# Kernel tuning notes

Measured on AMD Instinct MI355X. Metric: run time of the kernel, lower is better.

The kernel has to match this reference:

```python
import jax, jax.numpy as jnp
import numpy as np

B, S, D = 2, 2048, 2048
N_HEADS, N_KV_HEADS, HEAD_DIM = 16, 8, 128
N_REP = N_HEADS // N_KV_HEADS
EPS = 1e-6
SCALE = HEAD_DIM ** -0.5


def setup_inputs() -> dict:
    key = jax.random.key(0)
    ks = jax.random.split(key, 6)
    x = jax.random.normal(ks[0], (B, S, D), dtype=jnp.float32)
    # RoPE frequencies (Llama-style cis stored as interleaved [cos, sin])
    inv_freq = 1.0 / (1e6 ** (jnp.arange(0, HEAD_DIM, 2, dtype=jnp.float32) / HEAD_DIM))
    angles = jnp.arange(S, dtype=jnp.float32)[:, None] * inv_freq[None, :]  # [S, HEAD_DIM//2]
    freqs_cis = jnp.stack([jnp.cos(angles), jnp.sin(angles)], axis=-1)  # [S, HEAD_DIM//2, 2]
    wq = jax.random.normal(ks[1], (N_HEADS * HEAD_DIM, D), dtype=jnp.float32) * 0.02
    wk = jax.random.normal(ks[2], (N_KV_HEADS * HEAD_DIM, D), dtype=jnp.float32) * 0.02
    wv = jax.random.normal(ks[3], (N_KV_HEADS * HEAD_DIM, D), dtype=jnp.float32) * 0.02
    wo = jax.random.normal(ks[4], (D, N_HEADS * HEAD_DIM), dtype=jnp.float32) * 0.02
    q_norm_w = jnp.ones((HEAD_DIM,), dtype=jnp.float32)
    k_norm_w = jnp.ones((HEAD_DIM,), dtype=jnp.float32)
    return {"x": x, "freqs_cis": freqs_cis, "wq": wq, "wk": wk, "wv": wv,
            "wo": wo, "q_norm_w": q_norm_w, "k_norm_w": k_norm_w}


def _rmsnorm(t, w):
    var = jnp.mean(jnp.square(t), axis=-1, keepdims=True)
    return t * jax.lax.rsqrt(var + EPS) * w


def _apply_rope(t, cos, sin):
    # t: [B, S, H, HEAD_DIM]; cos/sin: [1, S, 1, HEAD_DIM//2]
    tp = t.reshape(*t.shape[:-1], HEAD_DIM // 2, 2)
    tr, ti = tp[..., 0], tp[..., 1]
    out = jnp.stack([tr * cos - ti * sin, tr * sin + ti * cos], axis=-1)
    return out.reshape(t.shape)


def reference(x, freqs_cis, wq, wk, wv, wo, q_norm_w, k_norm_w):
    bs, seqlen, _ = x.shape
    xq = (x @ wq.T).reshape(bs, seqlen, N_HEADS, HEAD_DIM)
    xk = (x @ wk.T).reshape(bs, seqlen, N_KV_HEADS, HEAD_DIM)
    xv = (x @ wv.T).reshape(bs, seqlen, N_KV_HEADS, HEAD_DIM)
    # per-head RMSNorm (Qwen3)
    xq = _rmsnorm(xq, q_norm_w)
    xk = _rmsnorm(xk, k_norm_w)
    # rotary embedding
    cos = freqs_cis[:seqlen, :, 0][None, :, None, :]
    sin = freqs_cis[:seqlen, :, 1][None, :, None, :]
    xq = _apply_rope(xq, cos, sin)
    xk = _apply_rope(xk, cos, sin)
    # GQA: repeat kv heads
    keys = jnp.repeat(xk, N_REP, axis=2)    # [B, S, N_HEADS, HEAD_DIM]
    values = jnp.repeat(xv, N_REP, axis=2)
    q = xq.transpose(0, 2, 1, 3)   # [B, H, S, D]
    k = keys.transpose(0, 2, 1, 3)
    v = values.transpose(0, 2, 1, 3)
    scores = jnp.einsum("bhqd,bhkd->bhqk", q, k) * SCALE
    causal = jnp.tril(jnp.ones((seqlen, seqlen), dtype=bool))
    scores = jnp.where(causal[None, None], scores, jnp.finfo(scores.dtype).min)
    attn = jax.nn.softmax(scores, axis=-1)
    out = jnp.einsum("bhqk,bhkd->bhqd", attn, v)
    out = out.transpose(0, 2, 1, 3).reshape(bs, seqlen, N_HEADS * HEAD_DIM)
    return out @ wo.T
```

## Files before the change

kernel.cpp:

```cpp
#include <hip/hip_runtime.h>

#define B_ 2
#define S_ 2048
#define D_ 2048
#define NH 16
#define NKV 8
#define HD 128
#define SCALE 0.08838834764831845f
#define CEXP 0.1275255f
#define RTHR 62.733f

typedef unsigned short u16;
typedef __attribute__((ext_vector_type(8))) short short8;
typedef __attribute__((ext_vector_type(4))) float f32x4;
typedef __attribute__((ext_vector_type(16))) float f32x16;
typedef __attribute__((ext_vector_type(4))) int i32x4;
typedef __attribute__((ext_vector_type(2))) int i32x2;

#define ASM_VMCNT(N) asm volatile("s_waitcnt vmcnt(" #N ")" ::: "memory")
#define LGKM0_FENCE asm volatile("s_waitcnt lgkmcnt(0)" ::: "memory")
#define MEMFENCE asm volatile("" ::: "memory")

__device__ __forceinline__ u16 f2b(float f) {
  union { float f; unsigned u; } c; c.f = f;
  unsigned u = c.u;
  return (u16)((u + 0x7fffu + ((u >> 16) & 1u)) >> 16);
}
__device__ __forceinline__ float b2f(u16 h) {
  union { unsigned u; float f; } c; c.u = ((unsigned)h) << 16;
  return c.f;
}
__device__ __forceinline__ float exp2f_fast(float x) {
  float r; asm("v_exp_f32 %0, %1" : "=v"(r) : "v"(x)); return r;
}
__device__ __forceinline__ int cvtpk(float a, float b) {
  int r; asm("v_cvt_pk_bf16_f32 %0, %1, %2" : "=v"(r) : "v"(a), "v"(b)); return r;
}
__device__ __forceinline__ void pl32swap(int& a, int& b) {
  asm volatile("v_permlane32_swap_b32 %0, %1" : "+v"(a), "+v"(b));
}

__device__ __forceinline__ void load_lds16(const u16* g, u16* l) {
  __builtin_amdgcn_global_load_lds(
      (const __attribute__((address_space(1))) unsigned int*)g,
      (__attribute__((address_space(3))) unsigned int*)l, 16, 0, 0);
}

__global__ __launch_bounds__(256) void cvt_all(const float* __restrict__ x,
                                               const float* __restrict__ wq,
                                               const float* __restrict__ wk,
                                               const float* __restrict__ wv,
                                               const float* __restrict__ wo,
                                               u16* __restrict__ xb,
                                               u16* __restrict__ wqkvb,
                                               u16* __restrict__ wob) {
  const int blk = blockIdx.x;
  const float* src; u16* dst; int base;
  if (blk < 8192)       { src = x;  dst = xb;                  base = blk; }
  else if (blk < 12288) { src = wq; dst = wqkvb;               base = blk - 8192; }
  else if (blk < 14336) { src = wk; dst = wqkvb + 2048 * 2048; base = blk - 12288; }
  else if (blk < 16384) { src = wv; dst = wqkvb + 3072 * 2048; base = blk - 14336; }
  else                  { src = wo; dst = wob;                 base = blk - 16384; }
  int i = base * 256 + threadIdx.x;
  float4 v = ((const float4*)src)[i];
  u16 o0 = f2b(v.x), o1 = f2b(v.y), o2 = f2b(v.z), o3 = f2b(v.w);
  unsigned long long packed = (unsigned long long)o0 | ((unsigned long long)o1 << 16) |
                              ((unsigned long long)o2 << 32) | ((unsigned long long)o3 << 48);
  ((unsigned long long*)dst)[i] = packed;
}

#define LDA4(dst, SRC, MI0) \
  { _Pragma("unroll") for (int i2 = 0; i2 < 4; ++i2) { \
      const int arow = wr * 128 + (MI0 + i2) * 16 + r; \
      dst[i2] = *(const short8*)&(SRC)[arow * 32 + ((hi ^ ((arow >> 1) & 3)) << 3)]; } }
#define LDB4(dst, SRC) \
  { _Pragma("unroll") for (int n2 = 0; n2 < 4; ++n2) { \
      const int brow = wc * 64 + n2 * 16 + r; \
      dst[n2] = *(const short8*)&(SRC)[brow * 32 + ((hi ^ ((brow >> 1) & 3)) << 3)]; } }
#define MFMA16(MI0, AF, BF) \
  { __builtin_amdgcn_s_setprio(1); \
    _Pragma("unroll") for (int i2 = 0; i2 < 4; ++i2) \
    _Pragma("unroll") for (int n2 = 0; n2 < 4; ++n2) \
      acc[MI0 + i2][n2] = __builtin_amdgcn_mfma_f32_16x16x32_bf16(AF[i2], BF[n2], acc[MI0 + i2][n2], 0, 0, 0); \
    __builtin_amdgcn_s_setprio(0); }

template<int OUTF32>
__global__ __launch_bounds__(512, 2) void gemm256(const u16* __restrict__ A, const u16* __restrict__ Bm,
                                                  void* __restrict__ Cv, int M, int N, int K, int nbn) {
  __shared__ __align__(16) u16 As[2][2][8192];
  __shared__ __align__(16) u16 Bs[2][2][8192];
  const int tid = threadIdx.x;
  const int wave = tid >> 6, lane = tid & 63;
  const int cpx = gridDim.x >> 3;
  const int L = (blockIdx.x & 7) * cpx + (blockIdx.x >> 3);
  const int bm = L / nbn, bn = L % nbn;
  const int wr = wave >> 2, wc = wave & 3;
  const int r = lane & 15, hi = lane >> 4;
  const int rowA0 = bm * 256, rowB0 = bn * 256;

  f32x4 acc[8][4];
#pragma unroll
  for (int mi = 0; mi < 8; ++mi)
#pragma unroll
    for (int ni = 0; ni < 4; ++ni) acc[mi][ni] = (f32x4){0.f, 0.f, 0.f, 0.f};

  auto stage_half = [&](const u16* G, int rowbase, u16* ldsb, int kcol) {
#pragma unroll
    for (int l = 0; l < 2; ++l) {
      const int p = wave * 2048 + l * 1024 + lane * 16;
      const int row = p >> 6, slot = (p >> 4) & 3;
      const int kg = slot ^ ((row >> 1) & 3);
      load_lds16(G + (size_t)(rowbase + row) * K + kcol + kg * 8,
                 ldsb + ((wave * 2048 + l * 1024) >> 1));
    }
  };

  stage_half(A,  rowA0, &As[0][0][0], 0);
  stage_half(Bm, rowB0, &Bs[0][0][0], 0);
  stage_half(A,  rowA0, &As[0][1][0], 32);
  stage_half(Bm, rowB0, &Bs[0][1][0], 32);
  ASM_VMCNT(4);
  __builtin_amdgcn_s_barrier();
  MEMFENCE;

  const int nk = K >> 6;
  for (int kt = 0; kt < nk; ++kt) {
    const int c = kt & 1, nb2 = c ^ 1;
    const int kn = (kt + 1) << 6;
    const bool hn = kt + 1 < nk;
    const u16* a0 = As[c][0]; const u16* b0 = Bs[c][0];
    const u16* a1 = As[c][1]; const u16* b1 = Bs[c][1];
    short8 af[4], bf[4];
    LDB4(bf, b0); LDA4(af, a0, 0);
    if (hn) stage_half(A, rowA0, &As[nb2][0][0], kn);
    __builtin_amdgcn_s_barrier();
    LGKM0_FENCE;
    MFMA16(0, af, bf);
    MEMFENCE;
    __builtin_amdgcn_s_barrier();
    LDA4(af, a0, 4);
    if (hn) { stage_half(Bm, rowB0, &Bs[nb2][0][0], kn); ASM_VMCNT(4); }
    else    { ASM_VMCNT(0); }
    __builtin_amdgcn_s_barrier();
    LGKM0_FENCE;
    MFMA16(4, af, bf);
    MEMFENCE;
    __builtin_amdgcn_s_barrier();
    LDB4(bf, b1); LDA4(af, a1, 0);
    if (hn) stage_half(A, rowA0, &As[nb2][1][0], kn + 32);
    __builtin_amdgcn_s_barrier();
    LGKM0_FENCE;
    MFMA16(0, af, bf);
    MEMFENCE;
    __builtin_amdgcn_s_barrier();
    LDA4(af, a1, 4);
    if (hn) { stage_half(Bm, rowB0, &Bs[nb2][1][0], kn + 32); ASM_VMCNT(4); }
    __builtin_amdgcn_s_barrier();
    LGKM0_FENCE;
    MFMA16(4, af, bf);
    MEMFENCE;
    __builtin_amdgcn_s_barrier();
  }

#pragma unroll
  for (int mi = 0; mi < 8; ++mi)
#pragma unroll
    for (int ni = 0; ni < 4; ++ni)
#pragma unroll
      for (int r2 = 0; r2 < 4; ++r2) {
        int grow = bm * 256 + wr * 128 + mi * 16 + hi * 4 + r2;
        int gcol = bn * 256 + wc * 64 + ni * 16 + r;
        if (OUTF32)
          ((float*)Cv)[(size_t)grow * N + gcol] = acc[mi][ni][r2];
        else
          ((u16*)Cv)[(size_t)grow * N + gcol] = f2b(acc[mi][ni][r2]);
      }
}

template<int OUTF32>
__global__ __launch_bounds__(256, 2) void gemm_bt2(const u16* __restrict__ A, const u16* __restrict__ Bm,
                                                   void* __restrict__ Cv, int M, int N, int K, int nbn) {
  __shared__ __align__(16) u16 As[2][128 * 64];
  __shared__ __align__(16) u16 Bs[2][128 * 64];
  const int tid = threadIdx.x;
  const int wave = tid >> 6, lane = tid & 63;
  const int nwg = gridDim.x, cpx = nwg >> 3;
  const int L = (blockIdx.x & 7) * cpx + (blockIdx.x >> 3);
  const int bm = L / nbn, bn = L % nbn;
  const int wr = wave >> 1, wc = wave & 1;
  const int r = lane & 15, hi = lane >> 4;

  f32x4 acc[4][4];
#pragma unroll
  for (int m = 0; m < 4; ++m)
#pragma unroll
    for (int n = 0; n < 4; ++n) acc[m][n] = (f32x4){0.f, 0.f, 0.f, 0.f};

  const int gslot = (lane & 7) ^ (lane >> 3);
  const int srow = lane >> 3;

  auto stage = [&](int buf, int k0) {
#pragma unroll
    for (int jj = 0; jj < 4; ++jj) {
      int j = wave * 4 + jj;
      int row = j * 8 + srow;
      load_lds16(A + (size_t)(bm * 128 + row) * K + k0 + gslot * 8, &As[buf][j * 512]);
      load_lds16(Bm + (size_t)(bn * 128 + row) * K + k0 + gslot * 8, &Bs[buf][j * 512]);
    }
  };

  const int nk = K >> 6;
  stage(0, 0);
  for (int kt = 0; kt < nk; ++kt) {
    if (kt + 1 < nk) {
      stage((kt + 1) & 1, (kt + 1) << 6);
      ASM_VMCNT(8);
    } else {
      ASM_VMCNT(0);
    }
    __builtin_amdgcn_s_barrier();
    MEMFENCE;
    const u16* as = As[kt & 1];
    const u16* bs = Bs[kt & 1];
#pragma unroll
    for (int kc = 0; kc < 2; ++kc) {
      short8 af[4], bfr[4];
#pragma unroll
      for (int m = 0; m < 4; ++m) {
        int row = wr * 64 + m * 16 + r;
        int slot = (hi + kc * 4) ^ (row & 7);
        af[m] = *(const short8*)&as[row * 64 + slot * 8];
      }
#pragma unroll
      for (int n = 0; n < 4; ++n) {
        int row = wc * 64 + n * 16 + r;
        int slot = (hi + kc * 4) ^ (row & 7);
        bfr[n] = *(const short8*)&bs[row * 64 + slot * 8];
      }
#pragma unroll
      for (int m = 0; m < 4; ++m)
#pragma unroll
        for (int n = 0; n < 4; ++n)
          acc[m][n] = __builtin_amdgcn_mfma_f32_16x16x32_bf16(af[m], bfr[n], acc[m][n], 0, 0, 0);
    }
    MEMFENCE;
    __builtin_amdgcn_s_barrier();
  }

#pragma unroll
  for (int m = 0; m < 4; ++m)
#pragma unroll
    for (int n = 0; n < 4; ++n)
#pragma unroll
      for (int r2 = 0; r2 < 4; ++r2) {
        int grow = bm * 128 + wr * 64 + m * 16 + hi * 4 + r2;
        int gcol = bn * 128 + wc * 64 + n * 16 + r;
        if (OUTF32)
          ((float*)Cv)[(size_t)grow * N + gcol] = acc[m][n][r2];
        else
          ((u16*)Cv)[(size_t)grow * N + gcol] = f2b(acc[m][n][r2]);
      }
}

__global__ __launch_bounds__(256) void rmsnorm_rope(const u16* __restrict__ qkv, const float* __restrict__ fc,
                                                    const float* __restrict__ qw, const float* __restrict__ kw,
                                                    u16* __restrict__ qr, u16* __restrict__ kr) {
  const int tid = threadIdx.x, wave = tid >> 6, lane = tid & 63;
  const int rowid = blockIdx.x * 4 + wave;
  const int token = rowid / 24;
  const int hh = rowid % 24;
  const int b = token >> 11, s = token & 2047;
  const bool isq = hh < 16;
  const int off = isq ? hh * 128 : 2048 + (hh - 16) * 128;
  const u16* src = qkv + (size_t)token * 4096 + off + lane * 2;
  unsigned pv = *(const unsigned*)src;
  float t0 = b2f((u16)(pv & 0xffffu));
  float t1 = b2f((u16)(pv >> 16));
  float ss = t0 * t0 + t1 * t1;
#pragma unroll
  for (int mm = 1; mm < 64; mm <<= 1) ss += __shfl_xor(ss, mm, 64);
  float rms = rsqrtf(ss * (1.0f / 128.0f) + 1e-6f);
  const float* nw = isq ? qw : kw;
  t0 *= rms * nw[lane * 2];
  t1 *= rms * nw[lane * 2 + 1];
  float c = fc[(s * 64 + lane) * 2], sn = fc[(s * 64 + lane) * 2 + 1];
  float o0 = t0 * c - t1 * sn;
  float o1 = t0 * sn + t1 * c;
  unsigned ov = (unsigned)f2b(o0) | ((unsigned)f2b(o1) << 16);
  if (isq)
    *(unsigned*)(qr + ((size_t)(b * 16 + hh) * 2048 + s) * 128 + lane * 2) = ov;
  else
    *(unsigned*)(kr + ((size_t)(b * 8 + hh - 16) * 2048 + s) * 128 + lane * 2) = ov;
}

__global__ __launch_bounds__(256) void v_transpose(const u16* __restrict__ qkv, u16* __restrict__ vt) {
  __shared__ __align__(16) u16 tile[64][136];
  const int blk = blockIdx.x;
  const int st = blk & 31, h = (blk >> 5) & 7, b = blk >> 8;
  const int s0 = st * 64, t = threadIdx.x;
#pragma unroll
  for (int p = 0; p < 4; ++p) {
    int row = p * 16 + (t >> 4), c8 = (t & 15) * 8;
    const u16* src = qkv + (size_t)(b * 2048 + s0 + row) * 4096 + 3072 + h * 128 + c8;
    *(short8*)&tile[row][c8] = *(const short8*)src;
  }
  __syncthreads();
  const int d = t >> 1, j0 = (t & 1) * 32;
  u16* dst = vt + ((size_t)(b * 8 + h) * 128 + d) * 2048 + s0 + j0;
#pragma unroll
  for (int j = 0; j < 32; j += 8) {
    short8 v;
#pragma unroll
    for (int u = 0; u < 8; ++u) v[u] = (short)tile[j0 + j + u][d];
    *(short8*)(dst + j) = v;
  }
}

__global__ __launch_bounds__(256, 2) void attn7(const u16* __restrict__ qr, const u16* __restrict__ kr,
                                                const u16* __restrict__ vt, u16* __restrict__ ao) {
  __shared__ __align__(16) u16 Ks[2][64 * 128];
  __shared__ __align__(16) u16 Vs[2][128 * 64];
  const int tid = threadIdx.x, wave = tid >> 6, lane = tid & 63;
  const int ql = lane & 31, lh = lane >> 5;

  const int blk = blockIdx.x;
  const int half = blk >> 8;
  const int xcd = blk & 7;
  const int idx = (blk >> 3) & 31;
  const int bh = xcd * 4 + (idx & 3);
  const int pp = idx >> 2;
  const int t = half ? pp : 15 - pp;
  const int b = bh >> 4, h = bh & 15, hkv = h >> 1;

  const u16* Q  = qr + (size_t)(b * 16 + h) * S_ * HD;
  const u16* Kg = kr + (size_t)(b * 8 + hkv) * S_ * HD;
  const u16* Vg = vt + (size_t)(b * 8 + hkv) * HD * S_;

  const int q0w = t * 128 + wave * 32;
  const int nsteps = 2 * (t + 1);

  short8 qf[8];
#pragma unroll
  for (int ki = 0; ki < 8; ++ki)
    qf[ki] = *(const short8*)(Q + (size_t)(q0w + ql) * HD + ki * 16 + lh * 8);

  f32x16 o[4];
#pragma unroll
  for (int dt = 0; dt < 4; ++dt) o[dt] = 0.f;
  float m = -1e30f, l = 0.f;

  auto stage = [&](int buf, int kv0) {
#pragma unroll
    for (int inst = 0; inst < 4; ++inst) {
      int pp2 = wave * 4096 + inst * 1024 + lane * 16;
      int row = pp2 >> 8;
      int colb = (pp2 & 255) ^ ((row & 7) << 4);
      load_lds16(Kg + (((size_t)(kv0 + row)) << 7) + (colb >> 1),
                 &Ks[buf][(wave * 4096 + inst * 1024) >> 1]);
    }
#pragma unroll
    for (int inst = 0; inst < 4; ++inst) {
      int pp2 = wave * 4096 + inst * 1024 + lane * 16;
      int d = pp2 >> 7;
      int colb = (pp2 & 127) ^ ((d & 7) << 4);
      load_lds16(Vg + (size_t)d * S_ + kv0 + (colb >> 1),
                 &Vs[buf][(wave * 4096 + inst * 1024) >> 1]);
    }
  };

  stage(0, 0);
  for (int i = 0; i < nsteps; ++i) {
    const int kv0 = i * 64;
    const u16* kb = Ks[i & 1];
    const u16* vb = Vs[i & 1];
    if (i + 1 < nsteps) {
      stage((i + 1) & 1, kv0 + 64);
      ASM_VMCNT(8);
    } else {
      ASM_VMCNT(0);
    }
    __builtin_amdgcn_s_barrier();
    MEMFENCE;

    if (kv0 < q0w + 32) {
      f32x16 sacc[2];
      sacc[0] = 0.f; sacc[1] = 0.f;
      __builtin_amdgcn_s_setprio(1);
#pragma unroll
      for (int ki = 0; ki < 8; ++ki) {
        const int off = ki * 32 + lh * 16;
#pragma unroll
        for (int kvt = 0; kvt < 2; ++kvt) {
          const int row = kvt * 32 + ql;
          short8 kf = *(const short8*)&kb[(row << 7) + ((off ^ ((row & 7) << 4)) >> 1)];
          sacc[kvt] = __builtin_amdgcn_mfma_f32_32x32x16_bf16(kf, qf[ki], sacc[kvt], 0, 0, 0);
        }
      }
      __builtin_amdgcn_s_setprio(0);
      const int q = q0w + ql;
      if (kv0 + 64 > q0w) {
#pragma unroll
        for (int kvt = 0; kvt < 2; ++kvt) {
          const int kvb = kv0 + kvt * 32 + 4 * lh;
#pragma unroll
          for (int reg = 0; reg < 16; ++reg) {
            const int kvr = kvb + (reg & 3) + 8 * (reg >> 2);
            sacc[kvt][reg] = (kvr > q) ? -1e30f : sacc[kvt][reg];
          }
        }
      }
      float mx = sacc[0][0];
#pragma unroll
      for (int kvt = 0; kvt < 2; ++kvt)
#pragma unroll
        for (int reg = 0; reg < 16; ++reg) mx = fmaxf(mx, sacc[kvt][reg]);
      mx = fmaxf(mx, __shfl_xor(mx, 32, 64));
      if (__any(mx > m + RTHR)) {
        float mn = fmaxf(m, mx);
        float sc = exp2f_fast((m - mn) * CEXP);
        l *= sc;
        m = mn;
#pragma unroll
        for (int dt = 0; dt < 4; ++dt)
#pragma unroll
          for (int reg = 0; reg < 16; ++reg) o[dt][reg] *= sc;
      }
      short8 pf[4];
      const float mc = m * CEXP;
      float ps = 0.f;
#pragma unroll
      for (int kvt = 0; kvt < 2; ++kvt) {
        float pv[16];
#pragma unroll
        for (int reg = 0; reg < 16; ++reg) {
          pv[reg] = exp2f_fast(__builtin_fmaf(sacc[kvt][reg], CEXP, -mc));
          ps += pv[reg];
        }
        int A0 = cvtpk(pv[0], pv[1]),  B0 = cvtpk(pv[2], pv[3]);
        int C0 = cvtpk(pv[4], pv[5]),  D0 = cvtpk(pv[6], pv[7]);
        int A1 = cvtpk(pv[8], pv[9]),  B1 = cvtpk(pv[10], pv[11]);
        int C1 = cvtpk(pv[12], pv[13]), D1 = cvtpk(pv[14], pv[15]);
        pl32swap(A0, C0);
        pl32swap(B0, D0);
        pl32swap(A1, C1);
        pl32swap(B1, D1);
        i32x4 w0 = (i32x4){A0, B0, C0, D0};
        i32x4 w1 = (i32x4){A1, B1, C1, D1};
        pf[kvt * 2]     = *(short8*)&w0;
        pf[kvt * 2 + 1] = *(short8*)&w1;
      }
      l += ps;
      __builtin_amdgcn_s_setprio(1);
#pragma unroll
      for (int kc = 0; kc < 4; ++kc) {
        const int off = kc * 32 + lh * 16;
#pragma unroll
        for (int dt = 0; dt < 4; ++dt) {
          const int d = dt * 32 + ql;
          short8 vf = *(const short8*)&vb[(d << 6) + ((off ^ ((d & 7) << 4)) >> 1)];
          o[dt] = __builtin_amdgcn_mfma_f32_32x32x16_bf16(vf, pf[kc], o[dt], 0, 0, 0);
        }
      }
      __builtin_amdgcn_s_setprio(0);
    }
    MEMFENCE;
    __builtin_amdgcn_s_barrier();
  }

  l += __shfl_xor(l, 32, 64);
  const float inv = 1.0f / l;
  const size_t rowoff = ((size_t)(b * 2048 + q0w + ql)) * 2048 + h * 128;
#pragma unroll
  for (int dt = 0; dt < 4; ++dt)
#pragma unroll
    for (int g = 0; g < 4; ++g) {
      const int d0 = dt * 32 + 8 * g + 4 * lh;
      int w0 = cvtpk(o[dt][4 * g] * inv, o[dt][4 * g + 1] * inv);
      int w1 = cvtpk(o[dt][4 * g + 2] * inv, o[dt][4 * g + 3] * inv);
      i32x2 pk = (i32x2){w0, w1};
      *(i32x2*)((u16*)ao + rowoff + d0) = pk;
    }
}

extern "C" void kernel_launch(void* const* d_in, const int* in_sizes, int n_in,
                              void* d_out, int out_size, void* d_ws, size_t ws_size,
                              hipStream_t stream) {
  const float* x = (const float*)d_in[0];
  const float* fc = (const float*)d_in[1];
  const float* wq = (const float*)d_in[2];
  const float* wk = (const float*)d_in[3];
  const float* wv = (const float*)d_in[4];
  const float* wo = (const float*)d_in[5];
  const float* qw = (const float*)d_in[6];
  const float* kw = (const float*)d_in[7];
  float* out = (float*)d_out;
  char* ws = (char*)d_ws;

  u16* xb    = (u16*)(ws);
  u16* wqkvb = (u16*)(ws + 16777216);
  u16* wob   = (u16*)(ws + 33554432);
  u16* qkv   = (u16*)(ws + 41943040);
  u16* qrope = (u16*)(ws + 75497472);
  u16* krope = (u16*)(ws + 92274688);
  u16* vtb   = (u16*)(ws + 100663296);
  u16* ao    = (u16*)(ws + 109051904);

  cvt_all<<<20480, 256, 0, stream>>>(x, wq, wk, wv, wo, xb, wqkvb, wob);

  gemm256<0><<<256, 512, 0, stream>>>(xb, wqkvb, (void*)qkv, 4096, 4096, 2048, 16);

  rmsnorm_rope<<<24576, 256, 0, stream>>>(qkv, fc, qw, kw, qrope, krope);
  v_transpose<<<512, 256, 0, stream>>>(qkv, vtb);

  attn7<<<512, 256, 0, stream>>>(qrope, krope, vtb, ao);

  gemm_bt2<1><<<512, 256, 0, stream>>>(ao, wob, (void*)out, 4096, 2048, 2048, 16);
}
```

Baseline: 211.5 us.

## Double-buffer GEMM register fragments to overlap LDS reads with MFMA

Restructures the GEMM main loop to use separate even/odd register fragment sets, so LDS reads for the next MFMA phase are issued before the current MFMA block runs. The explicit lgkmcnt(0) waits are removed and global-load waits are re-tuned, which shortens the chain of barrier-separated stalls. The cost is more register pressure, and the code now relies on the compiler to insert correct LDS wait counts. Reordering the stage_half calls also changes which buffer halves are in flight at each barrier, so correctness depends on the vmcnt values being right.

```diff
diff --git a/kernel.cpp b/kernel.cpp
--- a/kernel.cpp
+++ b/kernel.cpp
@@ -18,7 +18,6 @@
 typedef __attribute__((ext_vector_type(2))) int i32x2;
 
 #define ASM_VMCNT(N) asm volatile("s_waitcnt vmcnt(" #N ")" ::: "memory")
-#define LGKM0_FENCE asm volatile("s_waitcnt lgkmcnt(0)" ::: "memory")
 #define MEMFENCE asm volatile("" ::: "memory")
 
 __device__ __forceinline__ u16 f2b(float f) {
@@ -123,41 +122,46 @@
   __builtin_amdgcn_s_barrier();
   MEMFENCE;
 
+  short8 afE[4], afO[4], bfE[4], bfO[4];
+  LDB4(bfE, Bs[0][0]);
+  LDA4(afE, As[0][0], 0);
+
   const int nk = K >> 6;
   for (int kt = 0; kt < nk; ++kt) {
     const int c = kt & 1, nb2 = c ^ 1;
     const int kn = (kt + 1) << 6;
     const bool hn = kt + 1 < nk;
-    const u16* a0 = As[c][0]; const u16* b0 = Bs[c][0];
-    const u16* a1 = As[c][1]; const u16* b1 = Bs[c][1];
-    short8 af[4], bf[4];
-    LDB4(bf, b0); LDA4(af, a0, 0);
-    if (hn) stage_half(A, rowA0, &As[nb2][0][0], kn);
-    __builtin_amdgcn_s_barrier();
-    LGKM0_FENCE;
-    MFMA16(0, af, bf);
-    MEMFENCE;
-    __builtin_amdgcn_s_barrier();
-    LDA4(af, a0, 4);
-    if (hn) { stage_half(Bm, rowB0, &Bs[nb2][0][0], kn); ASM_VMCNT(4); }
+    LDA4(afO, As[c][0], 4);
+    if (hn) { stage_half(A, rowA0, &As[nb2][0][0], kn); ASM_VMCNT(2); }
     else    { ASM_VMCNT(0); }
-    __builtin_amdgcn_s_barrier();
-    LGKM0_FENCE;
-    MFMA16(4, af, bf);
-    MEMFENCE;
-    __builtin_amdgcn_s_barrier();
-    LDB4(bf, b1); LDA4(af, a1, 0);
-    if (hn) stage_half(A, rowA0, &As[nb2][1][0], kn + 32);
-    __builtin_amdgcn_s_barrier();
-    LGKM0_FENCE;
-    MFMA16(0, af, bf);
-    MEMFENCE;
-    __builtin_amdgcn_s_barrier();
-    LDA4(af, a1, 4);
-    if (hn) { stage_half(Bm, rowB0, &Bs[nb2][1][0], kn + 32); ASM_VMCNT(4); }
-    __builtin_amdgcn_s_barrier();
-    LGKM0_FENCE;
-    MFMA16(4, af, bf);
+    MEMFENCE;
+    __builtin_amdgcn_s_barrier();
+    MFMA16(0, afE, bfE);
+    MEMFENCE;
+    __builtin_amdgcn_s_barrier();
+    LDA4(afE, As[c][1], 0);
+    LDB4(bfO, Bs[c][1]);
+    if (hn) stage_half(Bm, rowB0, &Bs[nb2][0][0], kn);
+    MEMFENCE;
+    __builtin_amdgcn_s_barrier();
+    MFMA16(4, afO, bfE);
+    MEMFENCE;
+    __builtin_amdgcn_s_barrier();
+    LDA4(afO, As[c][1], 4);
+    if (hn) { stage_half(A, rowA0, &As[nb2][1][0], kn + 32); ASM_VMCNT(2); }
+    MEMFENCE;
+    __builtin_amdgcn_s_barrier();
+    MFMA16(0, afE, bfO);
+    MEMFENCE;
+    __builtin_amdgcn_s_barrier();
+    if (hn) {
+      LDA4(afE, As[nb2][0], 0);
+      LDB4(bfE, Bs[nb2][0]);
+      stage_half(Bm, rowB0, &Bs[nb2][1][0], kn + 32);
+    }
+    MEMFENCE;
+    __builtin_amdgcn_s_barrier();
+    MFMA16(4, afO, bfO);
     MEMFENCE;
     __builtin_amdgcn_s_barrier();
   }
```

Result: slower. 216.7 us (+2.4%).

## Replace QKV GEMM with 256x128-tile single-buffered kernel at higher occupancy

Applied to the files above, without the earlier changes.

The QKV projection GEMM changes from 256x256 tiles with a double-buffered, barrier-interleaved pipeline to 256x128 tiles over 512 blocks. Each k-step loads both 32-wide halves, waits on vmcnt(0), then runs the MFMAs. The smaller accumulator and LDS footprint allow launch bounds of 4 blocks per CU, and latency hiding is meant to come from other resident blocks rather than in-block prefetch. The cost is losing the global-load/compute overlap inside a block and more redundant A-tile loads.

```diff
diff --git a/kernel.cpp b/kernel.cpp
--- a/kernel.cpp
+++ b/kernel.cpp
@@ -18,7 +18,6 @@
 typedef __attribute__((ext_vector_type(2))) int i32x2;
 
 #define ASM_VMCNT(N) asm volatile("s_waitcnt vmcnt(" #N ")" ::: "memory")
-#define LGKM0_FENCE asm volatile("s_waitcnt lgkmcnt(0)" ::: "memory")
 #define MEMFENCE asm volatile("" ::: "memory")
 
 __device__ __forceinline__ u16 f2b(float f) {
@@ -69,111 +68,85 @@
   ((unsigned long long*)dst)[i] = packed;
 }
 
-#define LDA4(dst, SRC, MI0) \
+#define LDA4Q(dst, SRC) \
   { _Pragma("unroll") for (int i2 = 0; i2 < 4; ++i2) { \
-      const int arow = wr * 128 + (MI0 + i2) * 16 + r; \
+      const int arow = wr * 64 + i2 * 16 + r; \
       dst[i2] = *(const short8*)&(SRC)[arow * 32 + ((hi ^ ((arow >> 1) & 3)) << 3)]; } }
-#define LDB4(dst, SRC) \
+#define LDB4Q(dst, SRC) \
   { _Pragma("unroll") for (int n2 = 0; n2 < 4; ++n2) { \
       const int brow = wc * 64 + n2 * 16 + r; \
       dst[n2] = *(const short8*)&(SRC)[brow * 32 + ((hi ^ ((brow >> 1) & 3)) << 3)]; } }
-#define MFMA16(MI0, AF, BF) \
+#define MFMA16Q(AF, BF) \
   { __builtin_amdgcn_s_setprio(1); \
     _Pragma("unroll") for (int i2 = 0; i2 < 4; ++i2) \
     _Pragma("unroll") for (int n2 = 0; n2 < 4; ++n2) \
-      acc[MI0 + i2][n2] = __builtin_amdgcn_mfma_f32_16x16x32_bf16(AF[i2], BF[n2], acc[MI0 + i2][n2], 0, 0, 0); \
+      acc[i2][n2] = __builtin_amdgcn_mfma_f32_16x16x32_bf16(AF[i2], BF[n2], acc[i2][n2], 0, 0, 0); \
     __builtin_amdgcn_s_setprio(0); }
 
-template<int OUTF32>
-__global__ __launch_bounds__(512, 2) void gemm256(const u16* __restrict__ A, const u16* __restrict__ Bm,
-                                                  void* __restrict__ Cv, int M, int N, int K, int nbn) {
-  __shared__ __align__(16) u16 As[2][2][8192];
-  __shared__ __align__(16) u16 Bs[2][2][8192];
+__global__ __launch_bounds__(512, 4) void gemm256x128(const u16* __restrict__ A,
+                                                      const u16* __restrict__ Bm,
+                                                      u16* __restrict__ C) {
+  __shared__ __align__(16) u16 As2[2][8192];
+  __shared__ __align__(16) u16 Bs2[2][4096];
   const int tid = threadIdx.x;
   const int wave = tid >> 6, lane = tid & 63;
-  const int cpx = gridDim.x >> 3;
-  const int L = (blockIdx.x & 7) * cpx + (blockIdx.x >> 3);
-  const int bm = L / nbn, bn = L % nbn;
-  const int wr = wave >> 2, wc = wave & 3;
+  const int L = (blockIdx.x & 7) * 64 + (blockIdx.x >> 3);
+  const int bm = L >> 5, bn = L & 31;
+  const int wr = wave >> 1, wc = wave & 1;
   const int r = lane & 15, hi = lane >> 4;
-  const int rowA0 = bm * 256, rowB0 = bn * 256;
-
-  f32x4 acc[8][4];
-#pragma unroll
-  for (int mi = 0; mi < 8; ++mi)
+  const int rowA0 = bm * 256, rowB0 = bn * 128;
+
+  f32x4 acc[4][4];
+#pragma unroll
+  for (int mi = 0; mi < 4; ++mi)
 #pragma unroll
     for (int ni = 0; ni < 4; ++ni) acc[mi][ni] = (f32x4){0.f, 0.f, 0.f, 0.f};
 
-  auto stage_half = [&](const u16* G, int rowbase, u16* ldsb, int kcol) {
+  auto stage_ha = [&](u16* lds, int kcol) {
 #pragma unroll
     for (int l = 0; l < 2; ++l) {
       const int p = wave * 2048 + l * 1024 + lane * 16;
       const int row = p >> 6, slot = (p >> 4) & 3;
       const int kg = slot ^ ((row >> 1) & 3);
-      load_lds16(G + (size_t)(rowbase + row) * K + kcol + kg * 8,
-                 ldsb + ((wave * 2048 + l * 1024) >> 1));
+      load_lds16(A + (size_t)(rowA0 + row) * 2048 + kcol + kg * 8,
+                 lds + ((wave * 2048 + l * 1024) >> 1));
     }
   };
-
-  stage_half(A,  rowA0, &As[0][0][0], 0);
-  stage_half(Bm, rowB0, &Bs[0][0][0], 0);
-  stage_half(A,  rowA0, &As[0][1][0], 32);
-  stage_half(Bm, rowB0, &Bs[0][1][0], 32);
-  ASM_VMCNT(4);
-  __builtin_amdgcn_s_barrier();
-  MEMFENCE;
-
-  const int nk = K >> 6;
-  for (int kt = 0; kt < nk; ++kt) {
-    const int c = kt & 1, nb2 = c ^ 1;
-    const int kn = (kt + 1) << 6;
-    const bool hn = kt + 1 < nk;
-    const u16* a0 = As[c][0]; const u16* b0 = Bs[c][0];
-    const u16* a1 = As[c][1]; const u16* b1 = Bs[c][1];
+  auto stage_hb = [&](u16* lds, int kcol) {
+    const int p = wave * 1024 + lane * 16;
+    const int row = p >> 6, slot = (p >> 4) & 3;
+    const int kg = slot ^ ((row >> 1) & 3);
+    load_lds16(Bm + (size_t)(rowB0 + row) * 2048 + kcol + kg * 8,
+               lds + ((wave * 1024) >> 1));
+  };
+
+  for (int kt = 0; kt < 32; ++kt) {
+    const int k0 = kt << 6;
+    stage_ha(As2[0], k0);
+    stage_hb(Bs2[0], k0);
+    stage_ha(As2[1], k0 + 32);
+    stage_hb(Bs2[1], k0 + 32);
+    ASM_VMCNT(0);
+    __builtin_amdgcn_s_barrier();
+    MEMFENCE;
     short8 af[4], bf[4];
-    LDB4(bf, b0); LDA4(af, a0, 0);
-    if (hn) stage_half(A, rowA0, &As[nb2][0][0], kn);
-    __builtin_amdgcn_s_barrier();
-    LGKM0_FENCE;
-    MFMA16(0, af, bf);
-    MEMFENCE;
-    __builtin_amdgcn_s_barrier();
-    LDA4(af, a0, 4);
-    if (hn) { stage_half(Bm, rowB0, &Bs[nb2][0][0], kn); ASM_VMCNT(4); }
-    else    { ASM_VMCNT(0); }
-    __builtin_amdgcn_s_barrier();
-    LGKM0_FENCE;
-    MFMA16(4, af, bf);
-    MEMFENCE;
-    __builtin_amdgcn_s_barrier();
-    LDB4(bf, b1); LDA4(af, a1, 0);
-    if (hn) stage_half(A, rowA0, &As[nb2][1][0], kn + 32);
-    __builtin_amdgcn_s_barrier();
-    LGKM0_FENCE;
-    MFMA16(0, af, bf);
-    MEMFENCE;
-    __builtin_amdgcn_s_barrier();
-    LDA4(af, a1, 4);
-    if (hn) { stage_half(Bm, rowB0, &Bs[nb2][1][0], kn + 32); ASM_VMCNT(4); }
-    __builtin_amdgcn_s_barrier();
-    LGKM0_FENCE;
-    MFMA16(4, af, bf);
+    LDB4Q(bf, Bs2[0]); LDA4Q(af, As2[0]);
+    MFMA16Q(af, bf);
+    LDB4Q(bf, Bs2[1]); LDA4Q(af, As2[1]);
+    MFMA16Q(af, bf);
     MEMFENCE;
     __builtin_amdgcn_s_barrier();
   }
 
 #pragma unroll
-  for (int mi = 0; mi < 8; ++mi)
+  for (int mi = 0; mi < 4; ++mi)
 #pragma unroll
     for (int ni = 0; ni < 4; ++ni)
 #pragma unroll
       for (int r2 = 0; r2 < 4; ++r2) {
-        int grow = bm * 256 + wr * 128 + mi * 16 + hi * 4 + r2;
-        int gcol = bn * 256 + wc * 64 + ni * 16 + r;
-        if (OUTF32)
-          ((float*)Cv)[(size_t)grow * N + gcol] = acc[mi][ni][r2];
-        else
-          ((u16*)Cv)[(size_t)grow * N + gcol] = f2b(acc[mi][ni][r2]);
+        int grow = bm * 256 + wr * 64 + mi * 16 + hi * 4 + r2;
+        int gcol = bn * 128 + wc * 64 + ni * 16 + r;
+        C[(size_t)grow * 4096 + gcol] = f2b(acc[mi][ni][r2]);
       }
 }
 
@@ -507,7 +480,7 @@
 
   cvt_all<<<20480, 256, 0, stream>>>(x, wq, wk, wv, wo, xb, wqkvb, wob);
 
-  gemm256<0><<<256, 512, 0, stream>>>(xb, wqkvb, (void*)qkv, 4096, 4096, 2048, 16);
+  gemm256x128<<<512, 512, 0, stream>>>(xb, wqkvb, qkv);
 
   rmsnorm_rope<<<24576, 256, 0, stream>>>(qkv, fc, qw, kw, qrope, krope);
   v_transpose<<<512, 256, 0, stream>>>(qkv, vtb);
```

Measured after the change: 209.5 us. About the same (-0.9%).
